# Performance work log

Hardware: AMD Instinct MI355X
Metric: run time of the kernel (lower is better)

The kernel has to match this reference:

```python
import jax, jax.numpy as jnp
import numpy as np

B, T, IN_DIM = 128, 512, 32
H = 256            # h_dim; bidirectional -> embedding_dim D = 2*H = 512
N_EMB = 1024
BETA = 0.25


def setup_inputs() -> dict:
    key = jax.random.key(0)
    ks = jax.random.split(key, 12)
    traj = jax.random.normal(ks[0], (B, T, IN_DIM), dtype=jnp.float32)
    # variable-length padding mask: ones up to length, zeros after
    lengths = jax.random.randint(ks[1], (B,), 1, T + 1)
    mask = (jnp.arange(T)[None, :] < lengths[:, None]).astype(jnp.int32)
    s_x = 1.0 / np.sqrt(H)
    def u(k, shape):
        return jax.random.uniform(k, shape, jnp.float32, -s_x, s_x)
    # PyTorch GRU param layout: W_ih [3H, in], W_hh [3H, H], biases [3H]
    Wx_f, Wh_f = u(ks[2], (3 * H, IN_DIM)), u(ks[3], (3 * H, H))
    bx_f, bh_f = u(ks[4], (3 * H,)), u(ks[5], (3 * H,))
    Wx_b, Wh_b = u(ks[6], (3 * H, IN_DIM)), u(ks[7], (3 * H, H))
    bx_b, bh_b = u(ks[8], (3 * H,)), u(ks[9], (3 * H,))
    # codebook: nn.Embedding(n_embeddings, D) with uniform(-1/n, 1/n) init
    codebook = jax.random.uniform(ks[10], (N_EMB, 2 * H), jnp.float32,
                                  -1.0 / N_EMB, 1.0 / N_EMB)
    return {"traj": traj, "mask": mask,
            "Wx_f": Wx_f, "Wh_f": Wh_f, "bx_f": bx_f, "bh_f": bh_f,
            "Wx_b": Wx_b, "Wh_b": Wh_b, "bx_b": bx_b, "bh_b": bh_b,
            "codebook": codebook}


def _gru_dir(x, Wx, Wh, bx, bh):
    """Single-direction GRU over time (PyTorch gate math). x: [B,T,in] -> [B,T,H]."""
    b, t, _ = x.shape
    h_dim = Wh.shape[1]
    xg = jnp.einsum('bti,gi->btg', x, Wx) + bx  # precompute input gates [B,T,3H]
    def step(h, xg_t):
        hg = h @ Wh.T + bh
        xr, xz, xn = jnp.split(xg_t, 3, axis=-1)
        hr, hz, hn = jnp.split(hg, 3, axis=-1)
        r = jax.nn.sigmoid(xr + hr)
        z = jax.nn.sigmoid(xz + hz)
        n = jnp.tanh(xn + r * hn)
        h_new = (1.0 - z) * n + z * h
        return h_new, h_new
    h0 = jnp.zeros((b, h_dim), x.dtype)
    _, hs = jax.lax.scan(step, h0, jnp.swapaxes(xg, 0, 1))  # [T,B,H]
    return jnp.swapaxes(hs, 0, 1)


def _encode(traj, Wx_f, Wh_f, bx_f, bh_f, Wx_b, Wh_b, bx_b, bh_b):
    out_f = _gru_dir(traj, Wx_f, Wh_f, bx_f, bh_f)
    out_b = jnp.flip(_gru_dir(jnp.flip(traj, axis=1), Wx_b, Wh_b, bx_b, bh_b), axis=1)
    return jnp.concatenate([out_f, out_b], axis=-1)  # [B,T,2H]


def _vq(z_e, codebook, beta):
    # d(z, e) = |z|^2 + |e|^2 - 2 z.e  -> argmin over codebook
    d = (jnp.sum(z_e ** 2, axis=1, keepdims=True)
         + jnp.sum(codebook ** 2, axis=1)[None, :]
         - 2.0 * z_e @ codebook.T)                      # [B, N_EMB]
    idx = jnp.argmin(d, axis=1)                         # [B]
    z_q = codebook[idx]                                 # gather [B, D]
    loss = (jnp.mean((jax.lax.stop_gradient(z_q) - z_e) ** 2)
            + beta * jnp.mean((z_q - jax.lax.stop_gradient(z_e)) ** 2))
    z_q_st = z_e + jax.lax.stop_gradient(z_q - z_e)     # straight-through
    counts = jnp.zeros((codebook.shape[0],), z_e.dtype).at[idx].add(1.0)
    p = counts / z_e.shape[0]
    perplexity = jnp.exp(-jnp.sum(p * jnp.log(p + 1e-10)))
    return loss, z_q_st, perplexity, idx


def reference(traj, mask, Wx_f, Wh_f, bx_f, bh_f, Wx_b, Wh_b, bx_b, bh_b, codebook):
    z_e = _encode(traj, Wx_f, Wh_f, bx_f, bh_f, Wx_b, Wh_b, bx_b, bh_b)  # [B,T,2H]
    t = mask.shape[1]
    # last index where mask == 1:  T-1 - argmax(flip(mask))
    last_real_index = t - 1 - jnp.argmax(jnp.flip(mask, axis=1), axis=1)
    z_e_last = z_e[jnp.arange(z_e.shape[0]), last_real_index]            # [B,2H]
    loss, z_q, perplexity, _ = _vq(z_e_last, codebook, BETA)
    return z_q, loss, perplexity
```

## Files before the change

kernel.cpp:

```cpp
#include <hip/hip_runtime.h>
#include <math.h>

constexpr int B  = 128;
constexpr int T  = 512;
constexpr int IN = 32;
constexpr int H  = 256;
constexpr int D  = 2 * H;
constexpr int NC = 1024;

constexpr int NG   = 64;
constexpr int GW   = 4;
constexpr int SEQ  = 4;
constexpr int NTHR = 768;


__global__ void k_zero(int* __restrict__ counts, double* __restrict__ lsum) {
    const int i = blockIdx.x * 256 + threadIdx.x;
    if (i < NC) counts[i] = 0;
    if (i == 0) *lsum = 0.0;
}

__global__ void k_lengths(const int* __restrict__ mask, int* __restrict__ last) {
    const int b = blockIdx.x;
    const int t = threadIdx.x;
    int s = 0;
    #pragma unroll
    for (int m = 0; m < T / 64; ++m) s += mask[b * T + m * 64 + t];
    #pragma unroll
    for (int off = 32; off > 0; off >>= 1) s += __shfl_down(s, off, 64);
    if (t == 0) last[b] = s - 1;
}

__global__ void k_plan(const int* __restrict__ last, int* __restrict__ plan,
                       int* __restrict__ slen, int* __restrict__ glen) {
    __shared__ int ll[B];
    const int t = threadIdx.x;
    ll[t] = last[t];
    __syncthreads();
    const int lf = ll[t] + 1;
    const int lb = T - ll[t];
    int rf = 0, rb = 0;
    for (int j = 0; j < B; ++j) {
        const int ljf = ll[j] + 1, ljb = T - ll[j];
        rf += (ljf > lf) || (ljf == lf && j < t);
        rb += (ljb > lb) || (ljb == lb && j < t);
    }
    plan[rf] = t;       slen[rf] = lf;
    plan[128 + rb] = t; slen[128 + rb] = lb;
    if ((rf & 3) == 0) glen[rf >> 2] = lf;
    if ((rb & 3) == 0) glen[32 + (rb >> 2)] = lb;
}

__global__ void k_transpose(float* __restrict__ dst, const float* __restrict__ src,
                            int rows, int cols) {
    const int idx = blockIdx.x * 256 + threadIdx.x;
    const int r = idx % rows;
    const int c = idx / rows;
    dst[idx] = src[r * cols + c];
}

__global__ void k_cbn2(const float* __restrict__ cb, double* __restrict__ cbn2) {
    const int c = blockIdx.x * 256 + threadIdx.x;
    double s = 0.0;
    for (int k = 0; k < D; ++k) {
        const double e = (double)cb[c * D + k];
        s += e * e;
    }
    cbn2[c] = s;
}


__device__ __forceinline__ float sigmoidf_(float x) {
    return 1.0f / (1.0f + expf(-x));
}

__global__ __launch_bounds__(NTHR, 3) void k_gru(
    const float* __restrict__ traj,
    const float* __restrict__ Whf, const float* __restrict__ Whb,
    const float* __restrict__ Wxf, const float* __restrict__ Wxb,
    const float* __restrict__ bxf, const float* __restrict__ bhf,
    const float* __restrict__ bxb, const float* __restrict__ bhb,
    const int* __restrict__ plan, const int* __restrict__ slen,
    const int* __restrict__ glen,
    unsigned long long* __restrict__ hgt,
    float* __restrict__ ze)
{
    const int g   = blockIdx.x & 63;
    const int w   = blockIdx.x >> 6;
    const int dir = (g >= 32) ? 1 : 0;

    const float* __restrict__ Wh = dir ? Whb : Whf;
    const float* __restrict__ Wx = dir ? Wxb : Wxf;
    const float* __restrict__ bx = dir ? bxb : bxf;
    const float* __restrict__ bh = dir ? bhb : bhf;

    const int tid = threadIdx.x;
    const int kq  = tid / 96;
    const int rp  = tid - kq * 96;
    const int lr0 = 2 * rp;
    const int gi  = lr0 >> 6;
    const int Rg0 = gi * H + w * 64 + (lr0 & 63);

    __shared__ float4 h4[SEQ][64];
    __shared__ float  P [8][SEQ][194];
    __shared__ float  Px[8][SEQ][194];
    __shared__ float4 xb4[2][SEQ][8];
    __shared__ int    bbS[SEQ], lsS[SEQ];

    if (tid < SEQ) { bbS[tid] = plan[g * 4 + tid]; lsS[tid] = slen[g * 4 + tid]; }
    {
        float2* hp = (float2*)h4;
        if (tid < 512) hp[tid] = make_float2(0.0f, 0.0f);
    }
    const int L = glen[g];

    float4 wh[16];
    {
        const float4* p0 = (const float4*)(Wh + (size_t)Rg0 * 256 + kq * 32);
        const float4* p1 = (const float4*)(Wh + (size_t)(Rg0 + 1) * 256 + kq * 32);
        #pragma unroll
        for (int i = 0; i < 8; ++i) { wh[i] = p0[i]; wh[8 + i] = p1[i]; }
    }
    const float4 wx0 = *(const float4*)(Wx + Rg0 * 32 + kq * 4);
    const float4 wx1 = *(const float4*)(Wx + (Rg0 + 1) * 32 + kq * 4);

    float bxr = 0, bxz = 0, bxn = 0, bhr = 0, bhz = 0, bhn = 0;
    if (tid < 256) {
        const int j2 = tid & 63;
        bxr = bx[w * 64 + j2]; bxz = bx[H + w * 64 + j2]; bxn = bx[2 * H + w * 64 + j2];
        bhr = bh[w * 64 + j2]; bhz = bh[H + w * 64 + j2]; bhn = bh[2 * H + w * 64 + j2];
    }
    __syncthreads();
    if (tid < 128) {
        const int s = tid >> 5, i = tid & 31;
        const int t0 = dir ? (T - 1) : 0;
        ((float*)xb4)[128 + s * 32 + i] = traj[(bbS[s] * T + t0) * IN + i];
    }
    __syncthreads();

    const int u = tid - 256;

    for (int step = 1; step <= L; ++step) {
        const int buf = step & 1;
        unsigned long long* __restrict__ slab =
            hgt + (buf * NG + g) * (GW * SEQ * 64);

        float4 a0 = {0,0,0,0}, a1 = {0,0,0,0}, a2 = {0,0,0,0}, a3 = {0,0,0,0};
        float4 c0 = {0,0,0,0}, c1 = {0,0,0,0}, c2 = {0,0,0,0}, c3 = {0,0,0,0};
        #pragma unroll
        for (int i = 0; i < 8; ++i) {
            const float4 w0 = wh[i];
            const float4 w1 = wh[8 + i];
            float4 hv;
            hv = h4[0][kq * 8 + i];
            a0.x = fmaf(w0.x, hv.x, a0.x); a0.y = fmaf(w0.y, hv.y, a0.y);
            a0.z = fmaf(w0.z, hv.z, a0.z); a0.w = fmaf(w0.w, hv.w, a0.w);
            c0.x = fmaf(w1.x, hv.x, c0.x); c0.y = fmaf(w1.y, hv.y, c0.y);
            c0.z = fmaf(w1.z, hv.z, c0.z); c0.w = fmaf(w1.w, hv.w, c0.w);
            hv = h4[1][kq * 8 + i];
            a1.x = fmaf(w0.x, hv.x, a1.x); a1.y = fmaf(w0.y, hv.y, a1.y);
            a1.z = fmaf(w0.z, hv.z, a1.z); a1.w = fmaf(w0.w, hv.w, a1.w);
            c1.x = fmaf(w1.x, hv.x, c1.x); c1.y = fmaf(w1.y, hv.y, c1.y);
            c1.z = fmaf(w1.z, hv.z, c1.z); c1.w = fmaf(w1.w, hv.w, c1.w);
            hv = h4[2][kq * 8 + i];
            a2.x = fmaf(w0.x, hv.x, a2.x); a2.y = fmaf(w0.y, hv.y, a2.y);
            a2.z = fmaf(w0.z, hv.z, a2.z); a2.w = fmaf(w0.w, hv.w, a2.w);
            c2.x = fmaf(w1.x, hv.x, c2.x); c2.y = fmaf(w1.y, hv.y, c2.y);
            c2.z = fmaf(w1.z, hv.z, c2.z); c2.w = fmaf(w1.w, hv.w, c2.w);
            hv = h4[3][kq * 8 + i];
            a3.x = fmaf(w0.x, hv.x, a3.x); a3.y = fmaf(w0.y, hv.y, a3.y);
            a3.z = fmaf(w0.z, hv.z, a3.z); a3.w = fmaf(w0.w, hv.w, a3.w);
            c3.x = fmaf(w1.x, hv.x, c3.x); c3.y = fmaf(w1.y, hv.y, c3.y);
            c3.z = fmaf(w1.z, hv.z, c3.z); c3.w = fmaf(w1.w, hv.w, c3.w);
        }
        {
            float4 xv;
            float2 pv;
            xv = xb4[buf][0][kq];
            pv.x = a0.x + a0.y + a0.z + a0.w;
            pv.y = c0.x + c0.y + c0.z + c0.w;
            *(float2*)&P[kq][0][lr0] = pv;
            pv.x = wx0.x * xv.x + wx0.y * xv.y + wx0.z * xv.z + wx0.w * xv.w;
            pv.y = wx1.x * xv.x + wx1.y * xv.y + wx1.z * xv.z + wx1.w * xv.w;
            *(float2*)&Px[kq][0][lr0] = pv;
            xv = xb4[buf][1][kq];
            pv.x = a1.x + a1.y + a1.z + a1.w;
            pv.y = c1.x + c1.y + c1.z + c1.w;
            *(float2*)&P[kq][1][lr0] = pv;
            pv.x = wx0.x * xv.x + wx0.y * xv.y + wx0.z * xv.z + wx0.w * xv.w;
            pv.y = wx1.x * xv.x + wx1.y * xv.y + wx1.z * xv.z + wx1.w * xv.w;
            *(float2*)&Px[kq][1][lr0] = pv;
            xv = xb4[buf][2][kq];
            pv.x = a2.x + a2.y + a2.z + a2.w;
            pv.y = c2.x + c2.y + c2.z + c2.w;
            *(float2*)&P[kq][2][lr0] = pv;
            pv.x = wx0.x * xv.x + wx0.y * xv.y + wx0.z * xv.z + wx0.w * xv.w;
            pv.y = wx1.x * xv.x + wx1.y * xv.y + wx1.z * xv.z + wx1.w * xv.w;
            *(float2*)&Px[kq][2][lr0] = pv;
            xv = xb4[buf][3][kq];
            pv.x = a3.x + a3.y + a3.z + a3.w;
            pv.y = c3.x + c3.y + c3.z + c3.w;
            *(float2*)&P[kq][3][lr0] = pv;
            pv.x = wx0.x * xv.x + wx0.y * xv.y + wx0.z * xv.z + wx0.w * xv.w;
            pv.y = wx1.x * xv.x + wx1.y * xv.y + wx1.z * xv.z + wx1.w * xv.w;
            *(float2*)&Px[kq][3][lr0] = pv;
        }
        __syncthreads();

        if (tid < 256) {
            const int j2 = tid & 63, s = tid >> 6;
            float hr = 0.f, hz = 0.f, hn_ = 0.f, xr = 0.f, xz = 0.f, xn = 0.f;
            #pragma unroll
            for (int kk = 0; kk < 8; ++kk) {
                hr  += P [kk][s][j2];
                hz  += P [kk][s][64 + j2];
                hn_ += P [kk][s][128 + j2];
                xr  += Px[kk][s][j2];
                xz  += Px[kk][s][64 + j2];
                xn  += Px[kk][s][128 + j2];
            }
            const float r = sigmoidf_(xr + bxr + hr + bhr);
            const float z = sigmoidf_(xz + bxz + hz + bhz);
            const float n = tanhf(xn + bxn + r * (hn_ + bhn));
            const int jg = w * 64 + j2;
            const float hp = ((const float*)h4)[s * 256 + jg];
            const float hnew = (1.0f - z) * n + z * hp;
            ((float*)h4)[s * 256 + jg] = hnew;
            union { float f; unsigned ui; } cv; cv.f = hnew;
            const unsigned long long pk =
                ((unsigned long long)(unsigned)step << 32) | cv.ui;
            __hip_atomic_store(&slab[w * 256 + s * 64 + j2], pk,
                               __ATOMIC_RELAXED, __HIP_MEMORY_SCOPE_AGENT);
            if (step == lsS[s]) ze[bbS[s] * D + dir * H + jg] = hnew;
        } else {
            float xval = 0.0f;
            int xs = 0, xi = 0;
            const bool do_x = (u < 128) && (step < L);
            if (do_x) {
                xs = u >> 5; xi = u & 31;
                const int tn = dir ? (T - 1 - step) : step;
                xval = traj[(bbS[xs] * T + tn) * IN + xi];
            }
            const int p0 = u >> 8;
            const int r2 = u & 255;
            const int s0 = r2 >> 6, j0 = r2 & 63;
            const int pw0 = p0 + (p0 >= w ? 1 : 0);
            unsigned long long* ad0 = &slab[pw0 * 256 + s0 * 64 + j0];
            if (u < 256) {
                const int pw1 = 2 + (2 >= w ? 1 : 0);
                unsigned long long* ad1 = &slab[pw1 * 256 + s0 * 64 + j0];
                unsigned long long v0 = 0, v1 = 0;
                bool d0 = false, d1 = false;
                do {
                    if (!d0) { v0 = __hip_atomic_load(ad0, __ATOMIC_RELAXED,
                                   __HIP_MEMORY_SCOPE_AGENT); d0 = ((int)(v0 >> 32) >= step); }
                    if (!d1) { v1 = __hip_atomic_load(ad1, __ATOMIC_RELAXED,
                                   __HIP_MEMORY_SCOPE_AGENT); d1 = ((int)(v1 >> 32) >= step); }
                } while (!(d0 && d1));
                union { unsigned ui; float f; } e0, e1;
                e0.ui = (unsigned)v0; e1.ui = (unsigned)v1;
                ((float*)h4)[s0 * 256 + pw0 * 64 + j0] = e0.f;
                ((float*)h4)[s0 * 256 + pw1 * 64 + j0] = e1.f;
            } else {
                unsigned long long v0;
                do {
                    v0 = __hip_atomic_load(ad0, __ATOMIC_RELAXED,
                                           __HIP_MEMORY_SCOPE_AGENT);
                } while ((int)(v0 >> 32) < step);
                union { unsigned ui; float f; } e0; e0.ui = (unsigned)v0;
                ((float*)h4)[s0 * 256 + pw0 * 64 + j0] = e0.f;
            }
            if (do_x)
                ((float*)xb4)[(buf ^ 1) * 128 + xs * 32 + xi] = xval;
        }
        __syncthreads();
    }
}


__global__ __launch_bounds__(256) void k_vq(
    const float* __restrict__ ze, const float* __restrict__ cbT,
    const float* __restrict__ cb, const double* __restrict__ cbn2,
    int* __restrict__ counts, double* __restrict__ lsum,
    float* __restrict__ out)
{
    __shared__ float lz[D];
    __shared__ double ds[256];
    __shared__ int cs[256];

    const int b = blockIdx.x;
    const int t = threadIdx.x;

    lz[t]       = ze[b * D + t];
    lz[t + 256] = ze[b * D + 256 + t];
    __syncthreads();

    double best = 1e300;
    int bc = 0;
    for (int m = 0; m < NC / 256; ++m) {
        const int c = m * 256 + t;
        double s2 = 0.0;
        #pragma unroll 4
        for (int k = 0; k < D; ++k)
            s2 += (double)lz[k] * (double)cbT[k * NC + c];
        const double dist = cbn2[c] - 2.0 * s2;
        if (dist < best) { best = dist; bc = c; }
    }
    ds[t] = best; cs[t] = bc;
    __syncthreads();
    for (int s = 128; s > 0; s >>= 1) {
        if (t < s) {
            if (ds[t + s] < ds[t] || (ds[t + s] == ds[t] && cs[t + s] < cs[t])) {
                ds[t] = ds[t + s]; cs[t] = cs[t + s];
            }
        }
        __syncthreads();
    }
    const int idx = cs[0];
    __syncthreads();

    if (t == 0) atomicAdd(&counts[idx], 1);

    double loc = 0.0;
    for (int jj = t; jj < D; jj += 256) {
        const float zev = lz[jj];
        const float zqv = cb[idx * D + jj];
        out[b * D + jj] = zev + (zqv - zev);
        const double df = (double)zqv - (double)zev;
        loc += df * df;
    }
    ds[t] = loc;
    __syncthreads();
    for (int s = 128; s > 0; s >>= 1) {
        if (t < s) ds[t] += ds[t + s];
        __syncthreads();
    }
    if (t == 0) atomicAdd(lsum, ds[0]);
}

__global__ void k_final(const int* __restrict__ counts,
                        const double* __restrict__ lsum,
                        float* __restrict__ out)
{
    __shared__ double ds[256];
    const int t = threadIdx.x;
    double s = 0.0;
    for (int c = t; c < NC; c += 256) {
        const double p = (double)counts[c] / (double)B;
        s += p * log(p + 1e-10);
    }
    ds[t] = s;
    __syncthreads();
    for (int r = 128; r > 0; r >>= 1) {
        if (t < r) ds[t] += ds[t + r];
        __syncthreads();
    }
    if (t == 0) {
        out[B * D]     = (float)(lsum[0] * 1.25 / (double)(B * D));
        out[B * D + 1] = (float)exp(-ds[0]);
    }
}


extern "C" void kernel_launch(void* const* d_in, const int* in_sizes, int n_in,
                              void* d_out, int out_size, void* d_ws, size_t ws_size,
                              hipStream_t stream) {
    const float* traj = (const float*)d_in[0];
    const int*   mask = (const int*)d_in[1];
    const float* Wxf  = (const float*)d_in[2];
    const float* Whf  = (const float*)d_in[3];
    const float* bxf  = (const float*)d_in[4];
    const float* bhf  = (const float*)d_in[5];
    const float* Wxb  = (const float*)d_in[6];
    const float* Whb  = (const float*)d_in[7];
    const float* bxb  = (const float*)d_in[8];
    const float* bhb  = (const float*)d_in[9];
    const float* cb   = (const float*)d_in[10];
    float* out = (float*)d_out;

    float* ws    = (float*)d_ws;
    float* cbT   = ws;
    float* zebuf = cbT + 524288;
    unsigned long long* hgt =
        (unsigned long long*)(zebuf + 65536);
    int*   last  = (int*)(hgt + 131072);
    int*   plan  = last + 128;
    int*   slen  = plan + 256;
    int*   glen  = slen + 256;
    int*   cnts  = glen + 64;
    double* cbn2 = (double*)(cnts + 1024 + 4);
    double* lsum = cbn2 + 1024;

    k_zero<<<dim3(4), dim3(256), 0, stream>>>(cnts, lsum);
    k_lengths<<<dim3(B), dim3(64), 0, stream>>>(mask, last);
    k_plan<<<dim3(1), dim3(B), 0, stream>>>(last, plan, slen, glen);

    k_transpose<<<dim3(2048), dim3(256), 0, stream>>>(cbT, cb, NC, D);
    k_cbn2<<<dim3(4), dim3(256), 0, stream>>>(cb, cbn2);

    k_gru<<<dim3(NG * GW), dim3(NTHR), 0, stream>>>(
        traj, Whf, Whb, Wxf, Wxb, bxf, bhf, bxb, bhb,
        plan, slen, glen, hgt, zebuf);

    k_vq<<<dim3(B), dim3(256), 0, stream>>>(zebuf, cbT, cb, cbn2, cnts, lsum, out);
    k_final<<<dim3(1), dim3(256), 0, stream>>>(cnts, lsum, out);
}
```

Baseline: 1.724 ms.

## Add fast sc0 polling mirror slab for cross-block GRU hidden-state exchange

Each GRU block now writes its step-tagged hidden values both to the original agent-scope atomic slab and to a mirror slab, using inline-asm sc0 stores. Consumers poll the mirror with sc0 loads and fall back to an agent-scope atomic load every fourth iteration. The aim is to cut the per-step inter-block handoff latency on the serial recurrence. The next-step input prefetch also moves from the waiting threads to the gate threads, and k_zero now clears both slabs, which adds a larger zeroing launch. The cache-coherence reasoning behind sc0 polling is subtle and may rely on the fallback path for correctness.

```diff
diff --git a/kernel.cpp b/kernel.cpp
--- a/kernel.cpp
+++ b/kernel.cpp
@@ -14,10 +14,35 @@
 constexpr int NTHR = 768;
 
 
-__global__ void k_zero(int* __restrict__ counts, double* __restrict__ lsum) {
+__device__ __forceinline__ unsigned long long ld_fast(const unsigned long long* p) {
+    unsigned long long v;
+    asm volatile("global_load_dwordx2 %0, %1, off sc0\n\t"
+                 "s_waitcnt vmcnt(0)"
+                 : "=v"(v) : "v"(p) : "memory");
+    return v;
+}
+
+__device__ __forceinline__ void ld_fast2(const unsigned long long* p0,
+                                         const unsigned long long* p1,
+                                         unsigned long long& v0,
+                                         unsigned long long& v1) {
+    asm volatile("global_load_dwordx2 %0, %2, off sc0\n\t"
+                 "global_load_dwordx2 %1, %3, off sc0\n\t"
+                 "s_waitcnt vmcnt(0)"
+                 : "=&v"(v0), "=&v"(v1) : "v"(p0), "v"(p1) : "memory");
+}
+
+__device__ __forceinline__ void st_fast(unsigned long long* p, unsigned long long v) {
+    asm volatile("global_store_dwordx2 %0, %1, off sc0" :: "v"(p), "v"(v) : "memory");
+}
+
+
+__global__ void k_zero(int* __restrict__ counts, double* __restrict__ lsum,
+                       unsigned long long* __restrict__ slabs) {
     const int i = blockIdx.x * 256 + threadIdx.x;
     if (i < NC) counts[i] = 0;
     if (i == 0) *lsum = 0.0;
+    slabs[i] = 0ull;
 }
 
 __global__ void k_lengths(const int* __restrict__ mask, int* __restrict__ last) {
@@ -83,6 +108,7 @@
     const int* __restrict__ plan, const int* __restrict__ slen,
     const int* __restrict__ glen,
     unsigned long long* __restrict__ hgt,
+    unsigned long long* __restrict__ hgtF,
     float* __restrict__ ze)
 {
     const int g   = blockIdx.x & 63;
@@ -142,8 +168,9 @@
 
     for (int step = 1; step <= L; ++step) {
         const int buf = step & 1;
-        unsigned long long* __restrict__ slab =
-            hgt + (buf * NG + g) * (GW * SEQ * 64);
+        const int slabOff = (buf * NG + g) * (GW * SEQ * 64);
+        unsigned long long* __restrict__ slab  = hgt  + slabOff;
+        unsigned long long* __restrict__ slabF = hgtF + slabOff;
 
         float4 a0 = {0,0,0,0}, a1 = {0,0,0,0}, a2 = {0,0,0,0}, a3 = {0,0,0,0};
         float4 c0 = {0,0,0,0}, c1 = {0,0,0,0}, c2 = {0,0,0,0}, c3 = {0,0,0,0};
@@ -209,6 +236,14 @@
 
         if (tid < 256) {
             const int j2 = tid & 63, s = tid >> 6;
+            float xval = 0.0f;
+            int xs = 0, xi = 0;
+            const bool do_x = (tid < 128) && (step < L);
+            if (do_x) {
+                xs = tid >> 5; xi = tid & 31;
+                const int tn = dir ? (T - 1 - step) : step;
+                xval = traj[(bbS[xs] * T + tn) * IN + xi];
+            }
             float hr = 0.f, hz = 0.f, hn_ = 0.f, xr = 0.f, xz = 0.f, xn = 0.f;
             #pragma unroll
             for (int kk = 0; kk < 8; ++kk) {
@@ -229,49 +264,63 @@
             union { float f; unsigned ui; } cv; cv.f = hnew;
             const unsigned long long pk =
                 ((unsigned long long)(unsigned)step << 32) | cv.ui;
+            st_fast(&slabF[w * 256 + s * 64 + j2], pk);
             __hip_atomic_store(&slab[w * 256 + s * 64 + j2], pk,
                                __ATOMIC_RELAXED, __HIP_MEMORY_SCOPE_AGENT);
             if (step == lsS[s]) ze[bbS[s] * D + dir * H + jg] = hnew;
+            if (do_x)
+                ((float*)xb4)[(buf ^ 1) * 128 + xs * 32 + xi] = xval;
         } else {
-            float xval = 0.0f;
-            int xs = 0, xi = 0;
-            const bool do_x = (u < 128) && (step < L);
-            if (do_x) {
-                xs = u >> 5; xi = u & 31;
-                const int tn = dir ? (T - 1 - step) : step;
-                xval = traj[(bbS[xs] * T + tn) * IN + xi];
-            }
             const int p0 = u >> 8;
             const int r2 = u & 255;
             const int s0 = r2 >> 6, j0 = r2 & 63;
             const int pw0 = p0 + (p0 >= w ? 1 : 0);
-            unsigned long long* ad0 = &slab[pw0 * 256 + s0 * 64 + j0];
+            const int off0 = pw0 * 256 + s0 * 64 + j0;
             if (u < 256) {
                 const int pw1 = 2 + (2 >= w ? 1 : 0);
-                unsigned long long* ad1 = &slab[pw1 * 256 + s0 * 64 + j0];
+                const int off1 = pw1 * 256 + s0 * 64 + j0;
                 unsigned long long v0 = 0, v1 = 0;
                 bool d0 = false, d1 = false;
-                do {
-                    if (!d0) { v0 = __hip_atomic_load(ad0, __ATOMIC_RELAXED,
-                                   __HIP_MEMORY_SCOPE_AGENT); d0 = ((int)(v0 >> 32) >= step); }
-                    if (!d1) { v1 = __hip_atomic_load(ad1, __ATOMIC_RELAXED,
-                                   __HIP_MEMORY_SCOPE_AGENT); d1 = ((int)(v1 >> 32) >= step); }
-                } while (!(d0 && d1));
+                int it = 0;
+                for (;;) {
+                    unsigned long long t0, t1;
+                    ld_fast2(&slabF[off0], &slabF[off1], t0, t1);
+                    if (!d0 && (int)(t0 >> 32) >= step) { v0 = t0; d0 = true; }
+                    if (!d1 && (int)(t1 >> 32) >= step) { v1 = t1; d1 = true; }
+                    if (d0 && d1) break;
+                    if ((++it & 3) == 0) {
+                        if (!d0) {
+                            t0 = __hip_atomic_load(&slab[off0], __ATOMIC_RELAXED,
+                                                   __HIP_MEMORY_SCOPE_AGENT);
+                            if ((int)(t0 >> 32) >= step) { v0 = t0; d0 = true; }
+                        }
+                        if (!d1) {
+                            t1 = __hip_atomic_load(&slab[off1], __ATOMIC_RELAXED,
+                                                   __HIP_MEMORY_SCOPE_AGENT);
+                            if ((int)(t1 >> 32) >= step) { v1 = t1; d1 = true; }
+                        }
+                        if (d0 && d1) break;
+                    }
+                }
                 union { unsigned ui; float f; } e0, e1;
                 e0.ui = (unsigned)v0; e1.ui = (unsigned)v1;
                 ((float*)h4)[s0 * 256 + pw0 * 64 + j0] = e0.f;
                 ((float*)h4)[s0 * 256 + pw1 * 64 + j0] = e1.f;
             } else {
                 unsigned long long v0;
-                do {
-                    v0 = __hip_atomic_load(ad0, __ATOMIC_RELAXED,
-                                           __HIP_MEMORY_SCOPE_AGENT);
-                } while ((int)(v0 >> 32) < step);
+                int it = 0;
+                for (;;) {
+                    v0 = ld_fast(&slabF[off0]);
+                    if ((int)(v0 >> 32) >= step) break;
+                    if ((++it & 3) == 0) {
+                        v0 = __hip_atomic_load(&slab[off0], __ATOMIC_RELAXED,
+                                               __HIP_MEMORY_SCOPE_AGENT);
+                        if ((int)(v0 >> 32) >= step) break;
+                    }
+                }
                 union { unsigned ui; float f; } e0; e0.ui = (unsigned)v0;
                 ((float*)h4)[s0 * 256 + pw0 * 64 + j0] = e0.f;
             }
-            if (do_x)
-                ((float*)xb4)[(buf ^ 1) * 128 + xs * 32 + xi] = xval;
         }
         __syncthreads();
     }
@@ -381,9 +430,10 @@
     float* ws    = (float*)d_ws;
     float* cbT   = ws;
     float* zebuf = cbT + 524288;
-    unsigned long long* hgt =
+    unsigned long long* hgt  =
         (unsigned long long*)(zebuf + 65536);
-    int*   last  = (int*)(hgt + 131072);
+    unsigned long long* hgtF = hgt + 131072;
+    int*   last  = (int*)(hgtF + 131072);
     int*   plan  = last + 128;
     int*   slen  = plan + 256;
     int*   glen  = slen + 256;
@@ -391,7 +441,7 @@
     double* cbn2 = (double*)(cnts + 1024 + 4);
     double* lsum = cbn2 + 1024;
 
-    k_zero<<<dim3(4), dim3(256), 0, stream>>>(cnts, lsum);
+    k_zero<<<dim3(1024), dim3(256), 0, stream>>>(cnts, lsum, hgt);
     k_lengths<<<dim3(B), dim3(64), 0, stream>>>(mask, last);
     k_plan<<<dim3(1), dim3(B), 0, stream>>>(last, plan, slen, glen);
 
@@ -400,7 +450,7 @@
 
     k_gru<<<dim3(NG * GW), dim3(NTHR), 0, stream>>>(
         traj, Whf, Whb, Wxf, Wxb, bxf, bhf, bxb, bhb,
-        plan, slen, glen, hgt, zebuf);
+        plan, slen, glen, hgt, hgtF, zebuf);
 
     k_vq<<<dim3(B), dim3(256), 0, stream>>>(zebuf, cbT, cb, cbn2, cnts, lsum, out);
     k_final<<<dim3(1), dim3(256), 0, stream>>>(cnts, lsum, out);
```

New measurement: 1.939 ms. 12.5% more time.

## Overlap peer hidden-state polling with partial recurrent matvec per slice

Applied to the files above, without the earlier changes.

The cross-block hidden-state exchange moves from the end of each step to the start of the next. Three dedicated waves poll peer slabs and publish per-slice readiness counters in LDS. Compute waves start the matvec on their own locally produced slice and spin on those counters before each peer slice, so the exchange latency overlaps with FMA work. The slab buffer is now zeroed in k_zero, the Wh register layout is reordered by slice, and the input projection is hoisted ahead of the matvec. This adds intra-workgroup spin-waits with s_sleep and extra LDS atomics, which could add latency or hurt occupancy.

```diff
diff --git a/kernel.cpp b/kernel.cpp
--- a/kernel.cpp
+++ b/kernel.cpp
@@ -14,10 +14,12 @@
 constexpr int NTHR = 768;
 
 
-__global__ void k_zero(int* __restrict__ counts, double* __restrict__ lsum) {
+__global__ void k_zero(int* __restrict__ counts, double* __restrict__ lsum,
+                       unsigned long long* __restrict__ slab) {
     const int i = blockIdx.x * 256 + threadIdx.x;
     if (i < NC) counts[i] = 0;
     if (i == 0) *lsum = 0.0;
+    slab[i] = 0ull;
 }
 
 __global__ void k_lengths(const int* __restrict__ mask, int* __restrict__ last) {
@@ -73,6 +75,10 @@
 __device__ __forceinline__ float sigmoidf_(float x) {
     return 1.0f / (1.0f + expf(-x));
 }
+
+#define FMA4(acc, wv, hv)                                                     \
+    acc.x = fmaf(wv.x, hv.x, acc.x); acc.y = fmaf(wv.y, hv.y, acc.y);         \
+    acc.z = fmaf(wv.z, hv.z, acc.z); acc.w = fmaf(wv.w, hv.w, acc.w);
 
 __global__ __launch_bounds__(NTHR, 3) void k_gru(
     const float* __restrict__ traj,
@@ -95,6 +101,7 @@
     const float* __restrict__ bh = dir ? bhb : bhf;
 
     const int tid = threadIdx.x;
+    const int wid = tid >> 6;
     const int kq  = tid / 96;
     const int rp  = tid - kq * 96;
     const int lr0 = 2 * rp;
@@ -106,8 +113,10 @@
     __shared__ float  Px[8][SEQ][194];
     __shared__ float4 xb4[2][SEQ][8];
     __shared__ int    bbS[SEQ], lsS[SEQ];
+    __shared__ int    cntL[4];
 
     if (tid < SEQ) { bbS[tid] = plan[g * 4 + tid]; lsS[tid] = slen[g * 4 + tid]; }
+    if (tid < 4) cntL[tid] = 0;
     {
         float2* hp = (float2*)h4;
         if (tid < 512) hp[tid] = make_float2(0.0f, 0.0f);
@@ -115,11 +124,15 @@
     const int L = glen[g];
 
     float4 wh[16];
-    {
-        const float4* p0 = (const float4*)(Wh + (size_t)Rg0 * 256 + kq * 32);
-        const float4* p1 = (const float4*)(Wh + (size_t)(Rg0 + 1) * 256 + kq * 32);
-        #pragma unroll
-        for (int i = 0; i < 8; ++i) { wh[i] = p0[i]; wh[8 + i] = p1[i]; }
+    #pragma unroll
+    for (int q = 0; q < 4; ++q) {
+        const int p = (w + q) & 3;
+        const float* r0 = Wh + (size_t)Rg0 * 256 + p * 64 + kq * 8;
+        wh[q * 4 + 0] = ((const float4*)r0)[0];
+        wh[q * 4 + 1] = ((const float4*)r0)[1];
+        const float* r1 = r0 + 256;
+        wh[q * 4 + 2] = ((const float4*)r1)[0];
+        wh[q * 4 + 3] = ((const float4*)r1)[1];
     }
     const float4 wx0 = *(const float4*)(Wx + Rg0 * 32 + kq * 4);
     const float4 wx1 = *(const float4*)(Wx + (Rg0 + 1) * 32 + kq * 4);
@@ -138,72 +151,108 @@
     }
     __syncthreads();
 
-    const int u = tid - 256;
-
     for (int step = 1; step <= L; ++step) {
         const int buf = step & 1;
-        unsigned long long* __restrict__ slab =
+        unsigned long long* __restrict__ slabP =
+            hgt + (((step - 1) & 1) * NG + g) * (GW * SEQ * 64);
+        unsigned long long* __restrict__ slabC =
             hgt + (buf * NG + g) * (GW * SEQ * 64);
+
+        if (wid >= 8 && wid < 11) {
+            const int pi   = wid - 8;
+            const int pw   = (w + 1 + pi) & 3;
+            const int lane = tid & 63;
+            unsigned long long* sp = slabP + pw * 256 + lane;
+            const int tg = step - 1;
+            unsigned long long v0 = 0, v1 = 0, v2 = 0, v3 = 0;
+            bool d0 = false, d1 = false, d2 = false, d3 = false;
+            do {
+                if (!d0) { v0 = __hip_atomic_load(sp,       __ATOMIC_RELAXED,
+                               __HIP_MEMORY_SCOPE_AGENT); d0 = ((int)(v0 >> 32) >= tg); }
+                if (!d1) { v1 = __hip_atomic_load(sp + 64,  __ATOMIC_RELAXED,
+                               __HIP_MEMORY_SCOPE_AGENT); d1 = ((int)(v1 >> 32) >= tg); }
+                if (!d2) { v2 = __hip_atomic_load(sp + 128, __ATOMIC_RELAXED,
+                               __HIP_MEMORY_SCOPE_AGENT); d2 = ((int)(v2 >> 32) >= tg); }
+                if (!d3) { v3 = __hip_atomic_load(sp + 192, __ATOMIC_RELAXED,
+                               __HIP_MEMORY_SCOPE_AGENT); d3 = ((int)(v3 >> 32) >= tg); }
+            } while (!(d0 && d1 && d2 && d3));
+            float* hb = (float*)h4;
+            union { unsigned ui; float f; } e;
+            e.ui = (unsigned)v0; hb[0 * 256 + pw * 64 + lane] = e.f;
+            e.ui = (unsigned)v1; hb[1 * 256 + pw * 64 + lane] = e.f;
+            e.ui = (unsigned)v2; hb[2 * 256 + pw * 64 + lane] = e.f;
+            e.ui = (unsigned)v3; hb[3 * 256 + pw * 64 + lane] = e.f;
+            if (lane == 0)
+                __hip_atomic_fetch_add(&cntL[pw], 1, __ATOMIC_RELEASE,
+                                       __HIP_MEMORY_SCOPE_WORKGROUP);
+        }
+
+        float2 xv = make_float2(0.0f, 0.0f);
+        int xs = 0, xi = 0;
+        const bool do_x = (wid == 11) && (step < L);
+        if (do_x) {
+            const int lane = tid & 63;
+            xs = lane >> 4; xi = lane & 15;
+            const int tn = dir ? (T - 1 - step) : step;
+            xv = ((const float2*)(traj + (size_t)(bbS[xs] * T + tn) * IN))[xi];
+        }
 
         float4 a0 = {0,0,0,0}, a1 = {0,0,0,0}, a2 = {0,0,0,0}, a3 = {0,0,0,0};
         float4 c0 = {0,0,0,0}, c1 = {0,0,0,0}, c2 = {0,0,0,0}, c3 = {0,0,0,0};
+
+        {
+            float4 xq; float2 pv;
+            xq = xb4[buf][0][kq];
+            pv.x = wx0.x * xq.x + wx0.y * xq.y + wx0.z * xq.z + wx0.w * xq.w;
+            pv.y = wx1.x * xq.x + wx1.y * xq.y + wx1.z * xq.z + wx1.w * xq.w;
+            *(float2*)&Px[kq][0][lr0] = pv;
+            xq = xb4[buf][1][kq];
+            pv.x = wx0.x * xq.x + wx0.y * xq.y + wx0.z * xq.z + wx0.w * xq.w;
+            pv.y = wx1.x * xq.x + wx1.y * xq.y + wx1.z * xq.z + wx1.w * xq.w;
+            *(float2*)&Px[kq][1][lr0] = pv;
+            xq = xb4[buf][2][kq];
+            pv.x = wx0.x * xq.x + wx0.y * xq.y + wx0.z * xq.z + wx0.w * xq.w;
+            pv.y = wx1.x * xq.x + wx1.y * xq.y + wx1.z * xq.z + wx1.w * xq.w;
+            *(float2*)&Px[kq][2][lr0] = pv;
+            xq = xb4[buf][3][kq];
+            pv.x = wx0.x * xq.x + wx0.y * xq.y + wx0.z * xq.z + wx0.w * xq.w;
+            pv.y = wx1.x * xq.x + wx1.y * xq.y + wx1.z * xq.z + wx1.w * xq.w;
+            *(float2*)&Px[kq][3][lr0] = pv;
+        }
+
         #pragma unroll
-        for (int i = 0; i < 8; ++i) {
-            const float4 w0 = wh[i];
-            const float4 w1 = wh[8 + i];
-            float4 hv;
-            hv = h4[0][kq * 8 + i];
-            a0.x = fmaf(w0.x, hv.x, a0.x); a0.y = fmaf(w0.y, hv.y, a0.y);
-            a0.z = fmaf(w0.z, hv.z, a0.z); a0.w = fmaf(w0.w, hv.w, a0.w);
-            c0.x = fmaf(w1.x, hv.x, c0.x); c0.y = fmaf(w1.y, hv.y, c0.y);
-            c0.z = fmaf(w1.z, hv.z, c0.z); c0.w = fmaf(w1.w, hv.w, c0.w);
-            hv = h4[1][kq * 8 + i];
-            a1.x = fmaf(w0.x, hv.x, a1.x); a1.y = fmaf(w0.y, hv.y, a1.y);
-            a1.z = fmaf(w0.z, hv.z, a1.z); a1.w = fmaf(w0.w, hv.w, a1.w);
-            c1.x = fmaf(w1.x, hv.x, c1.x); c1.y = fmaf(w1.y, hv.y, c1.y);
-            c1.z = fmaf(w1.z, hv.z, c1.z); c1.w = fmaf(w1.w, hv.w, c1.w);
-            hv = h4[2][kq * 8 + i];
-            a2.x = fmaf(w0.x, hv.x, a2.x); a2.y = fmaf(w0.y, hv.y, a2.y);
-            a2.z = fmaf(w0.z, hv.z, a2.z); a2.w = fmaf(w0.w, hv.w, a2.w);
-            c2.x = fmaf(w1.x, hv.x, c2.x); c2.y = fmaf(w1.y, hv.y, c2.y);
-            c2.z = fmaf(w1.z, hv.z, c2.z); c2.w = fmaf(w1.w, hv.w, c2.w);
-            hv = h4[3][kq * 8 + i];
-            a3.x = fmaf(w0.x, hv.x, a3.x); a3.y = fmaf(w0.y, hv.y, a3.y);
-            a3.z = fmaf(w0.z, hv.z, a3.z); a3.w = fmaf(w0.w, hv.w, a3.w);
-            c3.x = fmaf(w1.x, hv.x, c3.x); c3.y = fmaf(w1.y, hv.y, c3.y);
-            c3.z = fmaf(w1.z, hv.z, c3.z); c3.w = fmaf(w1.w, hv.w, c3.w);
+        for (int q = 0; q < 4; ++q) {
+            const int p = (w + q) & 3;
+            if (q) {
+                while (__hip_atomic_load(&cntL[p], __ATOMIC_ACQUIRE,
+                                         __HIP_MEMORY_SCOPE_WORKGROUP) < step)
+                    __builtin_amdgcn_s_sleep(1);
+            }
+            const int hb = p * 16 + kq * 2;
+            float4 hv0, hv1;
+            hv0 = h4[0][hb]; hv1 = h4[0][hb + 1];
+            FMA4(a0, wh[q * 4 + 0], hv0); FMA4(a0, wh[q * 4 + 1], hv1);
+            FMA4(c0, wh[q * 4 + 2], hv0); FMA4(c0, wh[q * 4 + 3], hv1);
+            hv0 = h4[1][hb]; hv1 = h4[1][hb + 1];
+            FMA4(a1, wh[q * 4 + 0], hv0); FMA4(a1, wh[q * 4 + 1], hv1);
+            FMA4(c1, wh[q * 4 + 2], hv0); FMA4(c1, wh[q * 4 + 3], hv1);
+            hv0 = h4[2][hb]; hv1 = h4[2][hb + 1];
+            FMA4(a2, wh[q * 4 + 0], hv0); FMA4(a2, wh[q * 4 + 1], hv1);
+            FMA4(c2, wh[q * 4 + 2], hv0); FMA4(c2, wh[q * 4 + 3], hv1);
+            hv0 = h4[3][hb]; hv1 = h4[3][hb + 1];
+            FMA4(a3, wh[q * 4 + 0], hv0); FMA4(a3, wh[q * 4 + 1], hv1);
+            FMA4(c3, wh[q * 4 + 2], hv0); FMA4(c3, wh[q * 4 + 3], hv1);
         }
         {
-            float4 xv;
             float2 pv;
-            xv = xb4[buf][0][kq];
-            pv.x = a0.x + a0.y + a0.z + a0.w;
-            pv.y = c0.x + c0.y + c0.z + c0.w;
+            pv.x = a0.x + a0.y + a0.z + a0.w; pv.y = c0.x + c0.y + c0.z + c0.w;
             *(float2*)&P[kq][0][lr0] = pv;
-            pv.x = wx0.x * xv.x + wx0.y * xv.y + wx0.z * xv.z + wx0.w * xv.w;
-            pv.y = wx1.x * xv.x + wx1.y * xv.y + wx1.z * xv.z + wx1.w * xv.w;
-            *(float2*)&Px[kq][0][lr0] = pv;
-            xv = xb4[buf][1][kq];
-            pv.x = a1.x + a1.y + a1.z + a1.w;
-            pv.y = c1.x + c1.y + c1.z + c1.w;
+            pv.x = a1.x + a1.y + a1.z + a1.w; pv.y = c1.x + c1.y + c1.z + c1.w;
             *(float2*)&P[kq][1][lr0] = pv;
-            pv.x = wx0.x * xv.x + wx0.y * xv.y + wx0.z * xv.z + wx0.w * xv.w;
-            pv.y = wx1.x * xv.x + wx1.y * xv.y + wx1.z * xv.z + wx1.w * xv.w;
-            *(float2*)&Px[kq][1][lr0] = pv;
-            xv = xb4[buf][2][kq];
-            pv.x = a2.x + a2.y + a2.z + a2.w;
-            pv.y = c2.x + c2.y + c2.z + c2.w;
+            pv.x = a2.x + a2.y + a2.z + a2.w; pv.y = c2.x + c2.y + c2.z + c2.w;
             *(float2*)&P[kq][2][lr0] = pv;
-            pv.x = wx0.x * xv.x + wx0.y * xv.y + wx0.z * xv.z + wx0.w * xv.w;
-            pv.y = wx1.x * xv.x + wx1.y * xv.y + wx1.z * xv.z + wx1.w * xv.w;
-            *(float2*)&Px[kq][2][lr0] = pv;
-            xv = xb4[buf][3][kq];
-            pv.x = a3.x + a3.y + a3.z + a3.w;
-            pv.y = c3.x + c3.y + c3.z + c3.w;
+            pv.x = a3.x + a3.y + a3.z + a3.w; pv.y = c3.x + c3.y + c3.z + c3.w;
             *(float2*)&P[kq][3][lr0] = pv;
-            pv.x = wx0.x * xv.x + wx0.y * xv.y + wx0.z * xv.z + wx0.w * xv.w;
-            pv.y = wx1.x * xv.x + wx1.y * xv.y + wx1.z * xv.z + wx1.w * xv.w;
-            *(float2*)&Px[kq][3][lr0] = pv;
         }
         __syncthreads();
 
@@ -229,49 +278,11 @@
             union { float f; unsigned ui; } cv; cv.f = hnew;
             const unsigned long long pk =
                 ((unsigned long long)(unsigned)step << 32) | cv.ui;
-            __hip_atomic_store(&slab[w * 256 + s * 64 + j2], pk,
+            __hip_atomic_store(&slabC[w * 256 + s * 64 + j2], pk,
                                __ATOMIC_RELAXED, __HIP_MEMORY_SCOPE_AGENT);
             if (step == lsS[s]) ze[bbS[s] * D + dir * H + jg] = hnew;
-        } else {
-            float xval = 0.0f;
-            int xs = 0, xi = 0;
-            const bool do_x = (u < 128) && (step < L);
-            if (do_x) {
-                xs = u >> 5; xi = u & 31;
-                const int tn = dir ? (T - 1 - step) : step;
-                xval = traj[(bbS[xs] * T + tn) * IN + xi];
-            }
-            const int p0 = u >> 8;
-            const int r2 = u & 255;
-            const int s0 = r2 >> 6, j0 = r2 & 63;
-            const int pw0 = p0 + (p0 >= w ? 1 : 0);
-            unsigned long long* ad0 = &slab[pw0 * 256 + s0 * 64 + j0];
-            if (u < 256) {
-                const int pw1 = 2 + (2 >= w ? 1 : 0);
-                unsigned long long* ad1 = &slab[pw1 * 256 + s0 * 64 + j0];
-                unsigned long long v0 = 0, v1 = 0;
-                bool d0 = false, d1 = false;
-                do {
-                    if (!d0) { v0 = __hip_atomic_load(ad0, __ATOMIC_RELAXED,
-                                   __HIP_MEMORY_SCOPE_AGENT); d0 = ((int)(v0 >> 32) >= step); }
-                    if (!d1) { v1 = __hip_atomic_load(ad1, __ATOMIC_RELAXED,
-                                   __HIP_MEMORY_SCOPE_AGENT); d1 = ((int)(v1 >> 32) >= step); }
-                } while (!(d0 && d1));
-                union { unsigned ui; float f; } e0, e1;
-                e0.ui = (unsigned)v0; e1.ui = (unsigned)v1;
-                ((float*)h4)[s0 * 256 + pw0 * 64 + j0] = e0.f;
-                ((float*)h4)[s0 * 256 + pw1 * 64 + j0] = e1.f;
-            } else {
-                unsigned long long v0;
-                do {
-                    v0 = __hip_atomic_load(ad0, __ATOMIC_RELAXED,
-                                           __HIP_MEMORY_SCOPE_AGENT);
-                } while ((int)(v0 >> 32) < step);
-                union { unsigned ui; float f; } e0; e0.ui = (unsigned)v0;
-                ((float*)h4)[s0 * 256 + pw0 * 64 + j0] = e0.f;
-            }
-            if (do_x)
-                ((float*)xb4)[(buf ^ 1) * 128 + xs * 32 + xi] = xval;
+        } else if (do_x) {
+            ((float2*)xb4)[(buf ^ 1) * 64 + xs * 16 + xi] = xv;
         }
         __syncthreads();
     }
@@ -391,7 +402,7 @@
     double* cbn2 = (double*)(cnts + 1024 + 4);
     double* lsum = cbn2 + 1024;
 
-    k_zero<<<dim3(4), dim3(256), 0, stream>>>(cnts, lsum);
+    k_zero<<<dim3(512), dim3(256), 0, stream>>>(cnts, lsum, hgt);
     k_lengths<<<dim3(B), dim3(64), 0, stream>>>(mask, last);
     k_plan<<<dim3(1), dim3(B), 0, stream>>>(last, plan, slen, glen);
 
```

After: 6.131 ms. 3.56x slower.
